# Kernel tuning notes

Hardware: AMD Instinct MI355X
Metric: run time of the kernel (lower is better)

The kernel has to match this reference:

```python
import jax, jax.numpy as jnp
import numpy as np

DIM = 128
HEADS = 8
DH = DIM // HEADS
WIN = (4, 4, 4)
TOPK = 4
EPS = 1e-6


def _ln(x, g, b):
    mu = jnp.mean(x, -1, keepdims=True)
    var = jnp.mean((x - mu) ** 2, -1, keepdims=True)
    return (x - mu) * jax.lax.rsqrt(var + EPS) * g + b


def _win3d(x, p1, p2, p3):
    # x: [B,S,H,W,C] -> [B, p1*p2*p3, Ms, Mh, Mw, C]
    B, S, H, W, C = x.shape
    Ms, Mh, Mw = S // p1, H // p2, W // p3
    x = x.reshape(B, p1, Ms, p2, Mh, p3, Mw, C)
    x = x.transpose(0, 1, 3, 5, 2, 4, 6, 7)
    return x.reshape(B, p1 * p2 * p3, Ms, Mh, Mw, C)


def setup_inputs() -> dict:
    key = jax.random.key(0)
    ks = jax.random.split(key, 20)

    def lin(k, din, dout):
        return jax.random.normal(k, (din, dout), jnp.float32) * 0.02

    return {
        "x_in": jax.random.normal(ks[0], (2, 128, 16, 32, 32), jnp.float32),
        "x_g_in": jax.random.normal(ks[1], (2, 128, 8, 16, 16), jnp.float32),
        # Atten (global branch)
        "qkv_w": lin(ks[2], DIM, 3 * DIM), "qkv_b": jnp.zeros((3 * DIM,), jnp.float32),
        "proj_w": lin(ks[3], DIM, DIM), "proj_b": jnp.zeros((DIM,), jnp.float32),
        # shared LayerNorm (self.norm1 is reused everywhere in the original)
        "ln_g": jnp.ones((DIM,), jnp.float32), "ln_b": jnp.zeros((DIM,), jnp.float32),
        # mlp (global branch FFN)
        "mlp_w1": lin(ks[4], DIM, 4 * DIM), "mlp_b1": jnp.zeros((4 * DIM,), jnp.float32),
        "mlp_w2": lin(ks[5], 4 * DIM, DIM), "mlp_b2": jnp.zeros((DIM,), jnp.float32),
        # TopkRouting
        "rq_w": lin(ks[6], DIM, DIM), "rq_b": jnp.zeros((DIM,), jnp.float32),
        "rk_w": lin(ks[7], DIM, DIM), "rk_b": jnp.zeros((DIM,), jnp.float32),
        # fused qkv over concatenated local+gathered-global tokens
        "gqkv_w": lin(ks[8], DIM, 3 * DIM), "gqkv_b": jnp.zeros((3 * DIM,), jnp.float32),
        "wo_w": lin(ks[9], DIM, DIM), "wo_b": jnp.zeros((DIM,), jnp.float32),
        # mlp2 (local branch FFN)
        "mlp2_w1": lin(ks[10], DIM, 4 * DIM), "mlp2_b1": jnp.zeros((4 * DIM,), jnp.float32),
        "mlp2_w2": lin(ks[11], 4 * DIM, DIM), "mlp2_b2": jnp.zeros((DIM,), jnp.float32),
    }


def reference(x_in, x_g_in, qkv_w, qkv_b, proj_w, proj_b, ln_g, ln_b,
              mlp_w1, mlp_b1, mlp_w2, mlp_b2, rq_w, rq_b, rk_w, rk_b,
              gqkv_w, gqkv_b, wo_w, wo_b, mlp2_w1, mlp2_b1, mlp2_w2, mlp2_b2):
    B, C, S, H, W = x_in.shape
    Ms, Mh, Mw = WIN
    p1, p2, p3 = S // Ms, H // Mh, W // Mw  # pads are zero for these shapes
    nw, w3l = p1 * p2 * p3, Ms * Mh * Mw
    scale = DIM ** -0.5  # BiLevelRoutingAttention.scale = dim**-0.5 (not per-head)

    x = jnp.transpose(x_in, (0, 2, 3, 4, 1))  # [B,S,H,W,C]
    shortcut_l = _win3d(x, p1, p2, p3).reshape(B, nw, w3l, C)

    # ---- global branch: full self-attention + FFN ----
    _, _, gS, gH, gW = x_g_in.shape
    gN = gS * gH * gW
    xg = jnp.transpose(x_g_in, (0, 2, 3, 4, 1)).reshape(B, gN, C)
    h = _ln(xg, ln_g, ln_b)
    qkv = (h @ qkv_w + qkv_b).reshape(B, gN, 3, HEADS, DH).transpose(2, 0, 3, 1, 4)
    q, k, v = qkv[0], qkv[1], qkv[2]
    a = jax.nn.softmax(jnp.einsum('bhnd,bhmd->bhnm', q, k) * DH ** -0.5, axis=-1)
    o = jnp.einsum('bhnm,bhmd->bhnd', a, v).transpose(0, 2, 1, 3).reshape(B, gN, C)
    xg = (o @ proj_w + proj_b) + xg
    xg4 = xg.reshape(B, gS, gH, gW, C)
    h = _ln(xg4, ln_g, ln_b)
    xg4 = xg4 + (jax.nn.gelu(h @ mlp_w1 + mlp_b1, approximate=False) @ mlp_w2 + mlp_b2)

    # ---- top-k window routing ----
    swg = _win3d(xg4, p1, p2, p3)  # [B,nw,gMs,gMh,gMw,C]
    w3g = swg.shape[2] * swg.shape[3] * swg.shape[4]
    g_win = swg.mean((2, 3, 4))  # [B,nw,C]
    qh = g_win @ rq_w + rq_b
    kh = g_win @ rk_w + rk_b
    logit = jnp.einsum('bnc,bmc->bnm', qh * scale, kh)
    _tvals, tidx = jax.lax.top_k(logit, TOPK)  # r_weight is computed but unused in the original forward

    # gather top-k global windows' tokens per local window
    gflat = swg.reshape(B, nw, w3g, C)
    gath = jax.vmap(lambda kv, idx: kv[idx])(gflat, tidx)  # [B,nw,topk,w3g,C]
    sc = jnp.concatenate([shortcut_l, gath.reshape(B, nw, TOPK * w3g, C)], axis=2)
    w3 = w3l + TOPK * w3g

    # ---- local+routed attention over concatenated tokens ----
    qkvp = _ln(sc, ln_g, ln_b) @ gqkv_w + gqkv_b
    qp, kp, vp = jnp.split(qkvp, 3, axis=-1)
    qp = qp.reshape(B, nw, w3, HEADS, DH)
    kp = kp.reshape(B, nw, w3, HEADS, DH)
    vp = vp.reshape(B, nw, w3, HEADS, DH)
    aw = jax.nn.softmax(jnp.einsum('bnqhd,bnkhd->bnhqk', qp * scale, kp), axis=-1)
    out = jnp.einsum('bnhqk,bnkhd->bnqhd', aw, vp).reshape(B, nw, w3, C)

    l = out[:, :, :w3l] @ wo_w + wo_b + shortcut_l
    l = l.reshape(B, p1, p2, p3, Ms, Mh, Mw, C).transpose(0, 1, 4, 2, 5, 3, 6, 7).reshape(B, S, H, W, C)
    l = l + (jax.nn.gelu(_ln(l, ln_g, ln_b) @ mlp2_w1 + mlp2_b1, approximate=False) @ mlp2_w2 + mlp2_b2)

    l_out = jnp.transpose(l, (0, 4, 1, 2, 3))
    g_out = jnp.transpose(xg4, (0, 4, 1, 2, 3))
    return (l_out, g_out)
```

## Files before the change

### kernel.cpp

```cpp
#include <hip/hip_runtime.h>
#include <hip/hip_bf16.h>
#include <math.h>

#define BATCH 2
#define CDIM 128
#define SS 16
#define HH_ 32
#define WW_ 32
#define NSP (SS*HH_*WW_)
#define GS 8
#define GH 16
#define GW 16
#define GN (GS*GH*GW)
#define HEADS 8
#define DH 16
#define NW 256
#define W3L 64
#define W3G 8
#define TOPK 4
#define W3 (W3L + TOPK*W3G)
#define LN_EPS 1e-6f
#define ROUTE_SCALE 0.08838834764831845f
#define GATTN_SCALE 0.25f

typedef short bshort8 __attribute__((ext_vector_type(8)));
typedef float f32x4 __attribute__((ext_vector_type(4)));

__device__ __forceinline__ unsigned short f2bf(float f) {
    unsigned int u = __float_as_uint(f);
    unsigned int r = (u + 0x7fffu + ((u >> 16) & 1u)) >> 16;
    return (unsigned short)r;
}
__device__ __forceinline__ float gelu_exact(float x) {
    float z = x * 0.70710678118654752f;
    float az = fabsf(z);
    float t = 1.0f / fmaf(0.3275911f, az, 1.0f);
    float poly = t * fmaf(t, fmaf(t, fmaf(t, fmaf(t, 1.061405429f, -1.453152027f),
                     1.421413741f), -0.284496736f), 0.254829592f);
    float e = __expf(-az * az);
    float erfv = 1.0f - poly * e;
    erfv = (z < 0.f) ? -erfv : erfv;
    return 0.5f * x * (1.0f + erfv);
}
__device__ __forceinline__ float shfl_sum32(float v) {
#pragma unroll
    for (int m = 16; m > 0; m >>= 1) v += __shfl_xor(v, m);
    return v;
}
__device__ __forceinline__ float shfl_sum16(float v) {
#pragma unroll
    for (int m = 8; m > 0; m >>= 1) v += __shfl_xor(v, m);
    return v;
}
__device__ __forceinline__ float shfl_sum8(float v) {
#pragma unroll
    for (int m = 4; m > 0; m >>= 1) v += __shfl_xor(v, m);
    return v;
}

__global__ __launch_bounds__(256) void k_wprep_all(const float* __restrict__ gqkv_w,
        const float* __restrict__ m2_w1, const float* __restrict__ m2_w2,
        const float* __restrict__ proj_w, const float* __restrict__ mlp_w1,
        const float* __restrict__ mlp_w2, const float* __restrict__ wo_w,
        const float* __restrict__ qkv_w,
        unsigned short* __restrict__ wt, unsigned short* __restrict__ w1t,
        unsigned short* __restrict__ w2t, unsigned short* __restrict__ projt,
        unsigned short* __restrict__ gw1t, unsigned short* __restrict__ gw2t,
        unsigned short* __restrict__ wot, unsigned short* __restrict__ qkvt) {
    int id = blockIdx.x * 256 + threadIdx.x;
    int frag = id >> 6, lane = id & 63;
    int l15 = lane & 15, quad = lane >> 4;
    const float* srcw; unsigned short* dstw; int KS, OUT, lf; float sc = 1.f;
    if (frag < 96)        { lf = frag;       srcw = gqkv_w; dstw = wt;    KS = 4;  OUT = 384; if ((lf >> 2) < 8) sc = ROUTE_SCALE; }
    else if (frag < 224)  { lf = frag - 96;  srcw = m2_w1;  dstw = w1t;   KS = 4;  OUT = 512; }
    else if (frag < 352)  { lf = frag - 224; srcw = m2_w2;  dstw = w2t;   KS = 16; OUT = 128; }
    else if (frag < 384)  { lf = frag - 352; srcw = proj_w; dstw = projt; KS = 4;  OUT = 128; }
    else if (frag < 512)  { lf = frag - 384; srcw = mlp_w1; dstw = gw1t;  KS = 4;  OUT = 512; }
    else if (frag < 640)  { lf = frag - 512; srcw = mlp_w2; dstw = gw2t;  KS = 16; OUT = 128; }
    else if (frag < 672)  { lf = frag - 640; srcw = wo_w;   dstw = wot;   KS = 4;  OUT = 128; }
    else                  { lf = frag - 672; srcw = qkv_w;  dstw = qkvt;  KS = 4;  OUT = 384; if ((lf >> 2) < 8) sc = GATTN_SCALE; }
    int ksh = (KS == 16) ? 4 : 2;
    int tile = lf >> ksh, ks = lf & (KS - 1);
    int n = tile * 16 + l15;
    int k0 = ks * 32 + quad * 8;
    const float* s = srcw + (size_t)k0 * OUT + n;
    unsigned short o[8];
#pragma unroll
    for (int e = 0; e < 8; e++) o[e] = f2bf(s[(size_t)e * OUT] * sc);
    unsigned short* d = dstw + ((size_t)lf * 64 + lane) * 8;
    *(ushort4*)d = *(ushort4*)&o[0];
    *(ushort4*)(d + 4) = *(ushort4*)&o[4];
}

__global__ __launch_bounds__(256) void k_gqkv_mfma(const float* __restrict__ xg_in,
        const unsigned short* __restrict__ qkvt, const float* __restrict__ qkv_b,
        const float* __restrict__ ln_g, const float* __restrict__ ln_b,
        float* __restrict__ xg, unsigned short* __restrict__ qgb,
        unsigned short* __restrict__ kgb, unsigned short* __restrict__ vgtb) {
    int blk = blockIdx.x; int b = blk >> 7; int n0 = (blk & 127) * 16;
    int t = threadIdx.x; int w = t >> 6; int lane = t & 63;
    int l15 = lane & 15, quad = lane >> 4;
    __shared__ __align__(16) float xs[16 * 132];
    __shared__ __align__(16) unsigned short h[16 * 136];
    f32x4 zero4 = {0.f, 0.f, 0.f, 0.f};

    {
        int c = t >> 1, j0 = (t & 1) * 8;
        const float* src = xg_in + ((size_t)(b * 128 + c)) * GN + n0 + j0;
        float4 v0 = *(const float4*)src;
        float4 v1 = *(const float4*)(src + 4);
        xs[(j0 + 0) * 132 + c] = v0.x; xs[(j0 + 1) * 132 + c] = v0.y;
        xs[(j0 + 2) * 132 + c] = v0.z; xs[(j0 + 3) * 132 + c] = v0.w;
        xs[(j0 + 4) * 132 + c] = v1.x; xs[(j0 + 5) * 132 + c] = v1.y;
        xs[(j0 + 6) * 132 + c] = v1.z; xs[(j0 + 7) * 132 + c] = v1.w;
    }
    __syncthreads();
    {
        int j = t >> 4, p = t & 15, c0 = p * 8;
        float vv[8]; float s1 = 0.f;
#pragma unroll
        for (int i = 0; i < 8; i++) { vv[i] = xs[j * 132 + c0 + i]; s1 += vv[i]; }
        s1 = shfl_sum16(s1);
        float mu = s1 * (1.0f / 128.0f);
        float s2 = 0.f;
#pragma unroll
        for (int i = 0; i < 8; i++) { float d = vv[i] - mu; s2 += d * d; }
        s2 = shfl_sum16(s2);
        float rs = rsqrtf(s2 * (1.0f / 128.0f) + LN_EPS);
        float* dst = xg + ((size_t)(b * GN) + n0 + j) * 128 + c0;
        *(float4*)dst = *(float4*)&vv[0];
        *(float4*)(dst + 4) = *(float4*)&vv[4];
        unsigned short hb[8];
#pragma unroll
        for (int i4 = 0; i4 < 2; i4++) {
            float4 g4 = *(const float4*)(ln_g + c0 + i4 * 4);
            float4 b4 = *(const float4*)(ln_b + c0 + i4 * 4);
            hb[i4 * 4 + 0] = f2bf((vv[i4 * 4 + 0] - mu) * rs * g4.x + b4.x);
            hb[i4 * 4 + 1] = f2bf((vv[i4 * 4 + 1] - mu) * rs * g4.y + b4.y);
            hb[i4 * 4 + 2] = f2bf((vv[i4 * 4 + 2] - mu) * rs * g4.z + b4.z);
            hb[i4 * 4 + 3] = f2bf((vv[i4 * 4 + 3] - mu) * rs * g4.w + b4.w);
        }
        *(ushort4*)&h[j * 136 + c0] = *(ushort4*)&hb[0];
        *(ushort4*)&h[j * 136 + c0 + 4] = *(ushort4*)&hb[4];
    }
    __syncthreads();

    bshort8 a[4];
#pragma unroll
    for (int ks = 0; ks < 4; ks++)
        a[ks] = *(const bshort8*)(h + l15 * 136 + ks * 32 + quad * 8);
    int bh_base = b * HEADS;
#pragma unroll
    for (int part = 0; part < 2; part++) {
#pragma unroll
        for (int which = 0; which < 2; which++) {
            int nt = 2 * w + which;
            f32x4 acc = zero4;
#pragma unroll
            for (int ks = 0; ks < 4; ks++) {
                bshort8 bfr = *(const bshort8*)(qkvt + (((size_t)(part * 8 + nt) * 4 + ks) * 64 + lane) * 8);
                acc = __builtin_amdgcn_mfma_f32_16x16x32_bf16(a[ks], bfr, acc, 0, 0, 0);
            }
            int ncol = part * 128 + nt * 16;
            float bias = qkv_b[ncol + l15] * (part == 0 ? GATTN_SCALE : 1.f);
            unsigned short* dst = (part == 0) ? qgb : kgb;
#pragma unroll
            for (int r = 0; r < 4; r++)
                dst[((size_t)(bh_base + nt) * GN + n0 + quad * 4 + r) * DH + l15] = f2bf(acc[r] + bias);
        }
    }
#pragma unroll
    for (int which = 0; which < 2; which++) {
        int mtv = 2 * w + which;
        f32x4 acc = zero4;
#pragma unroll
        for (int ks = 0; ks < 4; ks++) {
            bshort8 aw = *(const bshort8*)(qkvt + (((size_t)(16 + mtv) * 4 + ks) * 64 + lane) * 8);
            acc = __builtin_amdgcn_mfma_f32_16x16x32_bf16(aw, a[ks], acc, 0, 0, 0);
        }
#pragma unroll
        for (int r = 0; r < 4; r++) {
            float bias = qkv_b[256 + mtv * 16 + quad * 4 + r];
            vgtb[((size_t)(bh_base + mtv) * DH + quad * 4 + r) * GN + n0 + l15] = f2bf(acc[r] + bias);
        }
    }
}

__global__ __launch_bounds__(256) void k_gattn_mfma(const unsigned short* __restrict__ qgb,
        const unsigned short* __restrict__ kgb, const unsigned short* __restrict__ vgtb,
        float* __restrict__ og) {
    int blk = blockIdx.x;
    int bh = blk >> 7; int qt = (blk & 127) << 4;
    int b = bh >> 3, hh = bh & 7;
    int t = threadIdx.x; int w = t >> 6; int lane = t & 63;
    int col = lane & 15, quad = lane >> 4;
    __shared__ __align__(16) unsigned short Pbuf[4 * 16 * 40];
    __shared__ float po[4][64][4];
    __shared__ float pl[4][64][4];

    bshort8 aq = {0, 0, 0, 0, 0, 0, 0, 0};
    if (quad < 2)
        aq = *(const bshort8*)(qgb + ((size_t)bh * GN + qt + col) * DH + quad * 8);

    f32x4 o = {0.f, 0.f, 0.f, 0.f};
    float lsum[4] = {0.f, 0.f, 0.f, 0.f};
    const unsigned short* kb = kgb + (size_t)bh * GN * DH;
    const unsigned short* vb = vgtb + (size_t)bh * DH * GN;
    unsigned short* pb = Pbuf + w * (16 * 40);
    int row0 = quad * 4;
    int kbeg = w * 512;
    for (int kc = kbeg; kc < kbeg + 512; kc += 32) {
        bshort8 bk0 = {0, 0, 0, 0, 0, 0, 0, 0};
        bshort8 bk1 = {0, 0, 0, 0, 0, 0, 0, 0};
        if (quad < 2) {
            bk0 = *(const bshort8*)(kb + (size_t)(kc + col) * DH + quad * 8);
            bk1 = *(const bshort8*)(kb + (size_t)(kc + 16 + col) * DH + quad * 8);
        }
        f32x4 z = {0.f, 0.f, 0.f, 0.f};
        f32x4 s0 = __builtin_amdgcn_mfma_f32_16x16x32_bf16(aq, bk0, z, 0, 0, 0);
        f32x4 s1 = __builtin_amdgcn_mfma_f32_16x16x32_bf16(aq, bk1, z, 0, 0, 0);
        float p0[4], p1[4];
#pragma unroll
        for (int r = 0; r < 4; r++) {
            p0[r] = __expf(s0[r]); p1[r] = __expf(s1[r]);
            lsum[r] += p0[r] + p1[r];
        }
#pragma unroll
        for (int r = 0; r < 4; r++) {
            pb[(row0 + r) * 40 + col] = f2bf(p0[r]);
            pb[(row0 + r) * 40 + 16 + col] = f2bf(p1[r]);
        }
        bshort8 pA = *(const bshort8*)(pb + col * 40 + quad * 8);
        bshort8 bv = *(const bshort8*)(vb + (size_t)col * GN + kc + quad * 8);
        o = __builtin_amdgcn_mfma_f32_16x16x32_bf16(pA, bv, o, 0, 0, 0);
    }
#pragma unroll
    for (int r = 0; r < 4; r++) {
        float v = lsum[r];
        v += __shfl_xor(v, 1); v += __shfl_xor(v, 2);
        v += __shfl_xor(v, 4); v += __shfl_xor(v, 8);
        lsum[r] = v;
    }
#pragma unroll
    for (int r = 0; r < 4; r++) { po[w][lane][r] = o[r]; pl[w][lane][r] = lsum[r]; }
    __syncthreads();
    if (w == 0) {
#pragma unroll
        for (int r = 0; r < 4; r++) {
            float os = po[0][lane][r] + po[1][lane][r] + po[2][lane][r] + po[3][lane][r];
            float ls = pl[0][lane][r] + pl[1][lane][r] + pl[2][lane][r] + pl[3][lane][r];
            og[((size_t)(b * GN) + qt + quad * 4 + r) * 128 + hh * 16 + col] = os / ls;
        }
    }
}

__global__ __launch_bounds__(256) void k_gmlp_mfma(const float* __restrict__ og,
        const float* __restrict__ xg,
        const unsigned short* __restrict__ projt, const float* __restrict__ proj_b,
        const float* __restrict__ ln_g, const float* __restrict__ ln_b,
        const unsigned short* __restrict__ gw1t, const float* __restrict__ b1,
        const unsigned short* __restrict__ gw2t, const float* __restrict__ b2,
        float* __restrict__ xg4, float* __restrict__ gout) {
    int blk = blockIdx.x; int b = blk >> 7; int n0g = (blk & 127) * 16;
    int t = threadIdx.x; int w = t >> 6; int lane = t & 63;
    int l15 = lane & 15, quad = lane >> 4;
    __shared__ __align__(16) unsigned short ao[16 * 136];
    __shared__ __align__(16) float xs[16 * 132];
    __shared__ __align__(16) unsigned short h[16 * 136];
    __shared__ __align__(16) unsigned short h1[16 * 520];
    float* of32 = (float*)h1;
    f32x4 zero4 = {0.f, 0.f, 0.f, 0.f};

    {
        int j = t >> 4, p = t & 15, c0 = p * 8;
        size_t base = ((size_t)(b * GN) + n0g + j) * 128 + c0;
        float4 v0 = *(const float4*)(og + base);
        float4 v1 = *(const float4*)(og + base + 4);
        ushort4 u0 = { f2bf(v0.x), f2bf(v0.y), f2bf(v0.z), f2bf(v0.w) };
        ushort4 u1 = { f2bf(v1.x), f2bf(v1.y), f2bf(v1.z), f2bf(v1.w) };
        *(ushort4*)&ao[j * 136 + c0] = u0;
        *(ushort4*)&ao[j * 136 + c0 + 4] = u1;
        *(float4*)&xs[j * 132 + c0] = *(const float4*)(xg + base);
        *(float4*)&xs[j * 132 + c0 + 4] = *(const float4*)(xg + base + 4);
    }
    __syncthreads();

    {
        bshort8 a[4];
#pragma unroll
        for (int ks = 0; ks < 4; ks++)
            a[ks] = *(const bshort8*)(ao + l15 * 136 + ks * 32 + quad * 8);
#pragma unroll
        for (int nt = 0; nt < 2; nt++) {
            f32x4 acc = zero4;
#pragma unroll
            for (int ks = 0; ks < 4; ks++) {
                bshort8 bfr = *(const bshort8*)(projt + (((size_t)(w * 2 + nt) * 4 + ks) * 64 + lane) * 8);
                acc = __builtin_amdgcn_mfma_f32_16x16x32_bf16(a[ks], bfr, acc, 0, 0, 0);
            }
            int n0 = w * 32 + nt * 16;
            float bias = proj_b[n0 + l15];
#pragma unroll
            for (int r = 0; r < 4; r++) {
                int m = quad * 4 + r;
                xs[m * 132 + n0 + l15] += acc[r] + bias;
            }
        }
    }
    __syncthreads();

    {
        int j = t >> 4, p = t & 15, c0 = p * 8;
        float vv[8]; float s1 = 0.f;
#pragma unroll
        for (int i = 0; i < 8; i++) { vv[i] = xs[j * 132 + c0 + i]; s1 += vv[i]; }
        s1 = shfl_sum16(s1);
        float mu = s1 * (1.0f / 128.0f);
        float s2 = 0.f;
#pragma unroll
        for (int i = 0; i < 8; i++) { float d = vv[i] - mu; s2 += d * d; }
        s2 = shfl_sum16(s2);
        float rs = rsqrtf(s2 * (1.0f / 128.0f) + LN_EPS);
        unsigned short hb[8];
#pragma unroll
        for (int i4 = 0; i4 < 2; i4++) {
            float4 g4 = *(const float4*)(ln_g + c0 + i4 * 4);
            float4 b4 = *(const float4*)(ln_b + c0 + i4 * 4);
            hb[i4 * 4 + 0] = f2bf((vv[i4 * 4 + 0] - mu) * rs * g4.x + b4.x);
            hb[i4 * 4 + 1] = f2bf((vv[i4 * 4 + 1] - mu) * rs * g4.y + b4.y);
            hb[i4 * 4 + 2] = f2bf((vv[i4 * 4 + 2] - mu) * rs * g4.z + b4.z);
            hb[i4 * 4 + 3] = f2bf((vv[i4 * 4 + 3] - mu) * rs * g4.w + b4.w);
        }
        *(ushort4*)&h[j * 136 + c0] = *(ushort4*)&hb[0];
        *(ushort4*)&h[j * 136 + c0 + 4] = *(ushort4*)&hb[4];
    }
    __syncthreads();

    {
        bshort8 a[4];
#pragma unroll
        for (int ks = 0; ks < 4; ks++)
            a[ks] = *(const bshort8*)(h + l15 * 136 + ks * 32 + quad * 8);
#pragma unroll
        for (int nt = 0; nt < 8; nt++) {
            f32x4 acc = zero4;
#pragma unroll
            for (int ks = 0; ks < 4; ks++) {
                bshort8 bfr = *(const bshort8*)(gw1t + (((size_t)(w * 8 + nt) * 4 + ks) * 64 + lane) * 8);
                acc = __builtin_amdgcn_mfma_f32_16x16x32_bf16(a[ks], bfr, acc, 0, 0, 0);
            }
            int n0 = w * 128 + nt * 16;
            float bias = b1[n0 + l15];
#pragma unroll
            for (int r = 0; r < 4; r++)
                h1[(quad * 4 + r) * 520 + n0 + l15] = f2bf(gelu_exact(acc[r] + bias));
        }
    }
    __syncthreads();

    f32x4 acc2[2]; acc2[0] = zero4; acc2[1] = zero4;
#pragma unroll 4
    for (int ks = 0; ks < 16; ks++) {
        bshort8 a = *(const bshort8*)(h1 + l15 * 520 + ks * 32 + quad * 8);
#pragma unroll
        for (int nt = 0; nt < 2; nt++) {
            bshort8 bfr = *(const bshort8*)(gw2t + (((size_t)(w * 2 + nt) * 16 + ks) * 64 + lane) * 8);
            acc2[nt] = __builtin_amdgcn_mfma_f32_16x16x32_bf16(a, bfr, acc2[nt], 0, 0, 0);
        }
    }
    __syncthreads();

    {
#pragma unroll
        for (int nt = 0; nt < 2; nt++) {
            int n0 = w * 32 + nt * 16;
            float bias = b2[n0 + l15];
#pragma unroll
            for (int r = 0; r < 4; r++) {
                int m = quad * 4 + r;
                float ov = xs[m * 132 + n0 + l15] + acc2[nt][r] + bias;
                of32[m * 132 + n0 + l15] = ov;
                xg4[((size_t)(b * GN) + n0g + m) * 128 + n0 + l15] = ov;
            }
        }
    }
    __syncthreads();

    {
        int cw = t >> 1, hf = t & 1, j0 = hf * 8;
        float* dst = gout + ((size_t)(b * 128 + cw)) * GN + n0g + j0;
#pragma unroll
        for (int i4 = 0; i4 < 2; i4++) {
            float4 ov = { of32[(j0 + i4 * 4 + 0) * 132 + cw], of32[(j0 + i4 * 4 + 1) * 132 + cw],
                          of32[(j0 + i4 * 4 + 2) * 132 + cw], of32[(j0 + i4 * 4 + 3) * 132 + cw] };
            *(float4*)(dst + i4 * 4) = ov;
        }
    }
}

__global__ void k_routing_qk(const float* __restrict__ xg4,
                             const float* __restrict__ rq_w, const float* __restrict__ rq_b,
                             const float* __restrict__ rk_w, const float* __restrict__ rk_b,
                             float* __restrict__ qh, float* __restrict__ kh) {
    int wid = blockIdx.x; int b = wid / NW, n = wid % NW;
    int c = threadIdx.x;
    int i1 = n / 64, i2 = (n / 8) % 8, i3 = n % 8;
    __shared__ float g[CDIM];
    float s = 0.f;
#pragma unroll
    for (int j = 0; j < W3G; j++) {
        int ds = j >> 2, dh = (j >> 1) & 1, dw = j & 1;
        int gi = ((i1 * 2 + ds) * GH + (i2 * 2 + dh)) * GW + (i3 * 2 + dw);
        s += xg4[((size_t)(b * GN + gi)) * CDIM + c];
    }
    g[c] = s * (1.0f / W3G);
    __syncthreads();
    float aq = rq_b[c], ak = rk_b[c];
    for (int k = 0; k < CDIM; k++) { float gv = g[k]; aq = fmaf(gv, rq_w[k * CDIM + c], aq); ak = fmaf(gv, rk_w[k * CDIM + c], ak); }
    qh[(size_t)wid * CDIM + c] = aq;
    kh[(size_t)wid * CDIM + c] = ak;
}

__global__ void k_topk(const float* __restrict__ qh, const float* __restrict__ kh,
                       int* __restrict__ tidx) {
    int wid = blockIdx.x; int b = wid / NW;
    int m = threadIdx.x;
    __shared__ float q[CDIM];
    __shared__ float lv[NW];
    __shared__ int li[NW];
    if (m < CDIM) q[m] = qh[(size_t)wid * CDIM + m] * ROUTE_SCALE;
    __syncthreads();
    float acc = 0.f;
    const float* kr = kh + ((size_t)b * NW + m) * CDIM;
    for (int k = 0; k < CDIM; k++) acc = fmaf(q[k], kr[k], acc);
#pragma unroll
    for (int sel = 0; sel < TOPK; sel++) {
        lv[m] = acc; li[m] = m; __syncthreads();
#pragma unroll
        for (int s = 128; s > 0; s >>= 1) {
            if (m < s) {
                if (lv[m + s] > lv[m] || (lv[m + s] == lv[m] && li[m + s] < li[m])) {
                    lv[m] = lv[m + s]; li[m] = li[m + s];
                }
            }
            __syncthreads();
        }
        int best = li[0]; __syncthreads();
        if (m == best) acc = -1e30f;
        if (m == 0) tidx[wid * TOPK + sel] = best;
    }
}

__global__ __launch_bounds__(256) void k_lnsc_local(const float* __restrict__ x_in,
        const float* __restrict__ ln_g, const float* __restrict__ ln_b,
        unsigned short* __restrict__ lnsc) {
    int blk = blockIdx.x;
    int wt = blk & 1; int hh = (blk >> 1) & 31; int s = (blk >> 6) & 15; int b = blk >> 10;
    int w0 = wt * 16;
    int t = threadIdx.x;
    __shared__ float tile[16][132];
    {
        int c = t >> 1; int wq = (t & 1) * 8;
        const float* src = x_in + (((size_t)(b * 128 + c) * SS + s)) * 1024 + hh * 32 + w0 + wq;
        float4 v0 = *(const float4*)src;
        float4 v1 = *(const float4*)(src + 4);
        tile[wq + 0][c] = v0.x; tile[wq + 1][c] = v0.y; tile[wq + 2][c] = v0.z; tile[wq + 3][c] = v0.w;
        tile[wq + 4][c] = v1.x; tile[wq + 5][c] = v1.y; tile[wq + 6][c] = v1.z; tile[wq + 7][c] = v1.w;
    }
    __syncthreads();
    int w = t >> 4; int j = t & 15;
    float vals[8];
    float s1 = 0.f;
#pragma unroll
    for (int i = 0; i < 8; i++) { vals[i] = tile[w][j * 8 + i]; s1 += vals[i]; }
    s1 = shfl_sum16(s1);
    float mu = s1 * (1.0f / 128.0f);
    float s2 = 0.f;
#pragma unroll
    for (int i = 0; i < 8; i++) { float d = vals[i] - mu; s2 += d * d; }
    s2 = shfl_sum16(s2);
    float rs = rsqrtf(s2 * (1.0f / 128.0f) + LN_EPS);
    float4 g0 = *(const float4*)(ln_g + j * 8);
    float4 g1 = *(const float4*)(ln_g + j * 8 + 4);
    float4 b0 = *(const float4*)(ln_b + j * 8);
    float4 b1 = *(const float4*)(ln_b + j * 8 + 4);
    float gv[8] = { g0.x, g0.y, g0.z, g0.w, g1.x, g1.y, g1.z, g1.w };
    float bv[8] = { b0.x, b0.y, b0.z, b0.w, b1.x, b1.y, b1.z, b1.w };
    int ww = w0 + w;
    int n = (s >> 2) * 64 + (hh >> 2) * 8 + (ww >> 2);
    int slot = (s & 3) * 16 + (hh & 3) * 4 + (ww & 3);
    unsigned short* dst = lnsc + ((size_t)(b * NW + n) * W3 + slot) * 128 + j * 8;
    ushort4 u0, u1;
    u0.x = f2bf((vals[0] - mu) * rs * gv[0] + bv[0]);
    u0.y = f2bf((vals[1] - mu) * rs * gv[1] + bv[1]);
    u0.z = f2bf((vals[2] - mu) * rs * gv[2] + bv[2]);
    u0.w = f2bf((vals[3] - mu) * rs * gv[3] + bv[3]);
    u1.x = f2bf((vals[4] - mu) * rs * gv[4] + bv[4]);
    u1.y = f2bf((vals[5] - mu) * rs * gv[5] + bv[5]);
    u1.z = f2bf((vals[6] - mu) * rs * gv[6] + bv[6]);
    u1.w = f2bf((vals[7] - mu) * rs * gv[7] + bv[7]);
    *(ushort4*)dst = u0;
    *(ushort4*)(dst + 4) = u1;
}

__global__ __launch_bounds__(256) void k_lnsc_gath(const float* __restrict__ xg4,
        const int* __restrict__ tidx,
        const float* __restrict__ ln_g, const float* __restrict__ ln_b,
        unsigned short* __restrict__ lnsc) {
    int blk = blockIdx.x;
    int kk = blk & 3; int wn = blk >> 2;
    int b = wn >> 8;
    int g = tidx[wn * TOPK + kk];
    int gi1 = g >> 6, gi2 = (g >> 3) & 7, gi3 = g & 7;
    int t = threadIdx.x; int j = t >> 5, lj = t & 31;
    int ds = j >> 2, dh = (j >> 1) & 1, dw = j & 1;
    int gi = ((gi1 * 2 + ds) * GH + (gi2 * 2 + dh)) * GW + (gi3 * 2 + dw);
    float4 v = *(const float4*)(xg4 + ((size_t)(b * GN + gi)) * 128 + lj * 4);
    float s1 = shfl_sum32(v.x + v.y + v.z + v.w);
    float mu = s1 * (1.0f / 128.0f);
    float d0 = v.x - mu, d1 = v.y - mu, d2 = v.z - mu, d3 = v.w - mu;
    float s2 = shfl_sum32(d0 * d0 + d1 * d1 + d2 * d2 + d3 * d3);
    float rs = rsqrtf(s2 * (1.0f / 128.0f) + LN_EPS);
    float4 g4 = *(const float4*)(ln_g + lj * 4);
    float4 b4 = *(const float4*)(ln_b + lj * 4);
    ushort4 u;
    u.x = f2bf(d0 * rs * g4.x + b4.x);
    u.y = f2bf(d1 * rs * g4.y + b4.y);
    u.z = f2bf(d2 * rs * g4.z + b4.z);
    u.w = f2bf(d3 * rs * g4.w + b4.w);
    *(ushort4*)(lnsc + ((size_t)wn * W3 + 64 + kk * 8 + j) * 128 + lj * 4) = u;
}

__global__ __launch_bounds__(512, 4) void k_local_mfma(const unsigned short* __restrict__ lnsc,
        const unsigned short* __restrict__ wt, const float* __restrict__ gqkv_b,
        float* __restrict__ aout) {
    int wn = blockIdx.x;
    int t = threadIdx.x; int w = t >> 6; int lane = t & 63;
    int l15 = lane & 15, quad = lane >> 4;
    __shared__ __align__(16) unsigned short Qs[64 * 136];
    __shared__ __align__(16) unsigned short Ks2[96 * 136];
    __shared__ __align__(16) unsigned short Vts[128 * 104];
    __shared__ __align__(16) unsigned short Ps[8][16 * 40];

    const unsigned short* Xb = lnsc + (size_t)wn * W3 * 128;
    f32x4 zero4 = {0.f, 0.f, 0.f, 0.f};

    bshort8 qw[4], kw[4], vw[4];
#pragma unroll
    for (int ks = 0; ks < 4; ks++) {
        qw[ks] = *(const bshort8*)(wt + (((size_t)(0 + w) * 4 + ks) * 64 + lane) * 8);
        kw[ks] = *(const bshort8*)(wt + (((size_t)(8 + w) * 4 + ks) * 64 + lane) * 8);
        vw[ks] = *(const bshort8*)(wt + (((size_t)(16 + w) * 4 + ks) * 64 + lane) * 8);
    }
    float qbias = gqkv_b[w * 16 + l15] * ROUTE_SCALE;
    float kbias = gqkv_b[128 + w * 16 + l15];
    float vbias[4];
#pragma unroll
    for (int r = 0; r < 4; r++) vbias[r] = gqkv_b[256 + w * 16 + quad * 4 + r];

    for (int mt = 0; mt < 6; mt++) {
        bshort8 a[4];
#pragma unroll
        for (int ks = 0; ks < 4; ks++)
            a[ks] = *(const bshort8*)(Xb + (mt * 16 + l15) * 128 + ks * 32 + quad * 8);
        f32x4 acck = zero4;
        f32x4 accv = zero4;
#pragma unroll
        for (int ks = 0; ks < 4; ks++) {
            acck = __builtin_amdgcn_mfma_f32_16x16x32_bf16(a[ks], kw[ks], acck, 0, 0, 0);
            accv = __builtin_amdgcn_mfma_f32_16x16x32_bf16(vw[ks], a[ks], accv, 0, 0, 0);
        }
#pragma unroll
        for (int r = 0; r < 4; r++) {
            Ks2[(mt * 16 + quad * 4 + r) * 136 + w * 16 + l15] = f2bf(acck[r] + kbias);
            Vts[(w * 16 + quad * 4 + r) * 104 + mt * 16 + l15] = f2bf(accv[r] + vbias[r]);
        }
        if (mt < 4) {
            f32x4 accq = zero4;
#pragma unroll
            for (int ks = 0; ks < 4; ks++)
                accq = __builtin_amdgcn_mfma_f32_16x16x32_bf16(a[ks], qw[ks], accq, 0, 0, 0);
#pragma unroll
            for (int r = 0; r < 4; r++)
                Qs[(mt * 16 + quad * 4 + r) * 136 + w * 16 + l15] = f2bf(accq[r] + qbias);
        }
    }

    unsigned short* Pw = &Ps[w][0];
    bshort8 zfrag = {0, 0, 0, 0, 0, 0, 0, 0};
    int h = w;
    for (int mt = 0; mt < 4; mt++) {
        bshort8 aq = zfrag;
        if (quad < 2)
            aq = *(const bshort8*)(Qs + (mt * 16 + l15) * 136 + h * 16 + quad * 8);
        float rsum[4] = {0.f, 0.f, 0.f, 0.f};
        f32x4 oacc = zero4;
#pragma unroll
        for (int kc = 0; kc < 96; kc += 32) {
#pragma unroll
            for (int sub = 0; sub < 2; sub++) {
                int nt = (kc >> 4) + sub;
                bshort8 bk = zfrag;
                if (quad < 2)
                    bk = *(const bshort8*)(Ks2 + (nt * 16 + l15) * 136 + h * 16 + quad * 8);
                f32x4 s = __builtin_amdgcn_mfma_f32_16x16x32_bf16(aq, bk, zero4, 0, 0, 0);
#pragma unroll
                for (int r = 0; r < 4; r++) {
                    float p = __expf(s[r]);
                    rsum[r] += p;
                    Pw[(quad * 4 + r) * 40 + sub * 16 + l15] = f2bf(p);
                }
            }
            bshort8 ap = *(const bshort8*)(Pw + l15 * 40 + quad * 8);
            bshort8 bv = *(const bshort8*)(Vts + (h * 16 + l15) * 104 + kc + quad * 8);
            oacc = __builtin_amdgcn_mfma_f32_16x16x32_bf16(ap, bv, oacc, 0, 0, 0);
        }
#pragma unroll
        for (int r = 0; r < 4; r++) {
            float v = rsum[r];
            v += __shfl_xor(v, 1); v += __shfl_xor(v, 2);
            v += __shfl_xor(v, 4); v += __shfl_xor(v, 8);
            rsum[r] = v;
        }
#pragma unroll
        for (int r = 0; r < 4; r++)
            aout[((size_t)wn * W3L + mt * 16 + quad * 4 + r) * 128 + h * 16 + l15]
                = oacc[r] / rsum[r];
    }
}

__global__ __launch_bounds__(256) void k_wo_mfma(const float* __restrict__ aout,
        const unsigned short* __restrict__ wot, const float* __restrict__ wo_b,
        const float* __restrict__ x_in, float* __restrict__ lpre) {
    int blk = blockIdx.x; int T0 = blk * 32;
    int b = T0 >> 14; int sp0 = T0 & 16383;
    int t = threadIdx.x; int w = t >> 6; int lane = t & 63;
    int l15 = lane & 15, quad = lane >> 4;
    __shared__ __align__(16) unsigned short as2[32 * 136];
    __shared__ __align__(16) float xs[32 * 132];
    f32x4 zero4 = {0.f, 0.f, 0.f, 0.f};

    {
        int j = t >> 3, p = t & 7, c0 = p * 16;
        int sp = sp0 + j;
        int s = sp >> 10, hh = (sp >> 5) & 31, ww = sp & 31;
        int n = (s >> 2) * 64 + (hh >> 2) * 8 + (ww >> 2);
        int slot = (s & 3) * 16 + (hh & 3) * 4 + (ww & 3);
        const float* src = aout + (((size_t)(b * NW + n)) * W3L + slot) * 128 + c0;
#pragma unroll
        for (int i4 = 0; i4 < 4; i4++) {
            float4 v = *(const float4*)(src + i4 * 4);
            ushort4 u = { f2bf(v.x), f2bf(v.y), f2bf(v.z), f2bf(v.w) };
            *(ushort4*)&as2[j * 136 + c0 + i4 * 4] = u;
        }
    }
    {
        int c = t >> 1, half = t & 1, j0 = half * 16;
        const float* src = x_in + ((size_t)(b * 128 + c)) * 16384 + sp0 + j0;
#pragma unroll
        for (int i4 = 0; i4 < 4; i4++) {
            float4 v = *(const float4*)(src + i4 * 4);
            xs[(j0 + i4 * 4 + 0) * 132 + c] = v.x;
            xs[(j0 + i4 * 4 + 1) * 132 + c] = v.y;
            xs[(j0 + i4 * 4 + 2) * 132 + c] = v.z;
            xs[(j0 + i4 * 4 + 3) * 132 + c] = v.w;
        }
    }
    __syncthreads();

    bshort8 a[2][4];
#pragma unroll
    for (int mt = 0; mt < 2; mt++)
#pragma unroll
        for (int ks = 0; ks < 4; ks++)
            a[mt][ks] = *(const bshort8*)(as2 + (mt * 16 + l15) * 136 + ks * 32 + quad * 8);
#pragma unroll
    for (int nt = 0; nt < 2; nt++) {
        int n0 = w * 32 + nt * 16;
        f32x4 acc0 = zero4, acc1 = zero4;
#pragma unroll
        for (int ks = 0; ks < 4; ks++) {
            bshort8 bfr = *(const bshort8*)(wot + (((size_t)(w * 2 + nt) * 4 + ks) * 64 + lane) * 8);
            acc0 = __builtin_amdgcn_mfma_f32_16x16x32_bf16(a[0][ks], bfr, acc0, 0, 0, 0);
            acc1 = __builtin_amdgcn_mfma_f32_16x16x32_bf16(a[1][ks], bfr, acc1, 0, 0, 0);
        }
        float bias = wo_b[n0 + l15];
#pragma unroll
        for (int r = 0; r < 4; r++) {
            int m0 = quad * 4 + r;
            int m1 = 16 + quad * 4 + r;
            lpre[((size_t)T0 + m0) * 128 + n0 + l15] = acc0[r] + bias + xs[m0 * 132 + n0 + l15];
            lpre[((size_t)T0 + m1) * 128 + n0 + l15] = acc1[r] + bias + xs[m1 * 132 + n0 + l15];
        }
    }
}

__global__ __launch_bounds__(256) void k_mlp2_mfma(const float* __restrict__ lpre,
        const float* __restrict__ ln_g, const float* __restrict__ ln_b,
        const unsigned short* __restrict__ w1t, const float* __restrict__ b1,
        const unsigned short* __restrict__ w2t, const float* __restrict__ b2,
        float* __restrict__ lout) {
    int blk = blockIdx.x;
    int T0 = blk * 32;
    int b = T0 >> 14;
    int sp = T0 & 16383;
    int t = threadIdx.x; int w = t >> 6; int lane = t & 63;
    int l15 = lane & 15, quad = lane >> 4;
    __shared__ __align__(16) unsigned short buf[32 * 520];
    float* of32 = (float*)buf;

    float res[2][2][4];
#pragma unroll
    for (int mt = 0; mt < 2; mt++)
#pragma unroll
        for (int nt = 0; nt < 2; nt++)
#pragma unroll
            for (int r = 0; r < 4; r++)
                res[mt][nt][r] = lpre[((size_t)T0 + mt * 16 + quad * 4 + r) * 128 + w * 32 + nt * 16 + l15];

    {
        int j = t >> 3, p = t & 7, c0 = p * 16;
        const float* src = lpre + ((size_t)T0 + j) * 128 + c0;
        float4 v0 = *(const float4*)(src + 0);
        float4 v1 = *(const float4*)(src + 4);
        float4 v2 = *(const float4*)(src + 8);
        float4 v3 = *(const float4*)(src + 12);
        float s1 = (v0.x + v0.y + v0.z + v0.w) + (v1.x + v1.y + v1.z + v1.w)
                 + (v2.x + v2.y + v2.z + v2.w) + (v3.x + v3.y + v3.z + v3.w);
        s1 = shfl_sum8(s1);
        float mu = s1 * (1.0f / 128.0f);
        float vv[16] = { v0.x, v0.y, v0.z, v0.w, v1.x, v1.y, v1.z, v1.w,
                         v2.x, v2.y, v2.z, v2.w, v3.x, v3.y, v3.z, v3.w };
        float s2 = 0.f;
#pragma unroll
        for (int i = 0; i < 16; i++) { float d = vv[i] - mu; s2 += d * d; }
        s2 = shfl_sum8(s2);
        float rs = rsqrtf(s2 * (1.0f / 128.0f) + LN_EPS);
        unsigned short hb[16];
#pragma unroll
        for (int i4 = 0; i4 < 4; i4++) {
            float4 g4 = *(const float4*)(ln_g + c0 + i4 * 4);
            float4 b4 = *(const float4*)(ln_b + c0 + i4 * 4);
            hb[i4 * 4 + 0] = f2bf((vv[i4 * 4 + 0] - mu) * rs * g4.x + b4.x);
            hb[i4 * 4 + 1] = f2bf((vv[i4 * 4 + 1] - mu) * rs * g4.y + b4.y);
            hb[i4 * 4 + 2] = f2bf((vv[i4 * 4 + 2] - mu) * rs * g4.z + b4.z);
            hb[i4 * 4 + 3] = f2bf((vv[i4 * 4 + 3] - mu) * rs * g4.w + b4.w);
        }
        *(ushort4*)&buf[j * 136 + c0 + 0] = *(ushort4*)&hb[0];
        *(ushort4*)&buf[j * 136 + c0 + 4] = *(ushort4*)&hb[4];
        *(ushort4*)&buf[j * 136 + c0 + 8] = *(ushort4*)&hb[8];
        *(ushort4*)&buf[j * 136 + c0 + 12] = *(ushort4*)&hb[12];
    }
    __syncthreads();

    bshort8 a1[2][4];
#pragma unroll
    for (int mt = 0; mt < 2; mt++)
#pragma unroll
        for (int ks = 0; ks < 4; ks++)
            a1[mt][ks] = *(const bshort8*)(buf + (mt * 16 + l15) * 136 + ks * 32 + quad * 8);
    __syncthreads();

    f32x4 zero4 = {0.f, 0.f, 0.f, 0.f};
    {
#pragma unroll
        for (int nt = 0; nt < 8; nt++) {
            int n0 = w * 128 + nt * 16;
            f32x4 acc0 = zero4, acc1 = zero4;
#pragma unroll
            for (int ks = 0; ks < 4; ks++) {
                bshort8 bfr = *(const bshort8*)(w1t + (((size_t)(w * 8 + nt) * 4 + ks) * 64 + lane) * 8);
                acc0 = __builtin_amdgcn_mfma_f32_16x16x32_bf16(a1[0][ks], bfr, acc0, 0, 0, 0);
                acc1 = __builtin_amdgcn_mfma_f32_16x16x32_bf16(a1[1][ks], bfr, acc1, 0, 0, 0);
            }
            float bias = b1[n0 + l15];
#pragma unroll
            for (int r = 0; r < 4; r++) {
                buf[(quad * 4 + r) * 520 + n0 + l15] = f2bf(gelu_exact(acc0[r] + bias));
                buf[(16 + quad * 4 + r) * 520 + n0 + l15] = f2bf(gelu_exact(acc1[r] + bias));
            }
        }
    }
    __syncthreads();

    f32x4 acc[2][2];
    acc[0][0] = zero4; acc[0][1] = zero4; acc[1][0] = zero4; acc[1][1] = zero4;
    {
#pragma unroll 4
        for (int ks = 0; ks < 16; ks++) {
            bshort8 a0 = *(const bshort8*)(buf + (l15) * 520 + ks * 32 + quad * 8);
            bshort8 a1b = *(const bshort8*)(buf + (16 + l15) * 520 + ks * 32 + quad * 8);
#pragma unroll
            for (int nt = 0; nt < 2; nt++) {
                bshort8 bfr = *(const bshort8*)(w2t + (((size_t)(w * 2 + nt) * 16 + ks) * 64 + lane) * 8);
                acc[0][nt] = __builtin_amdgcn_mfma_f32_16x16x32_bf16(a0, bfr, acc[0][nt], 0, 0, 0);
                acc[1][nt] = __builtin_amdgcn_mfma_f32_16x16x32_bf16(a1b, bfr, acc[1][nt], 0, 0, 0);
            }
        }
    }
    __syncthreads();

#pragma unroll
    for (int mt = 0; mt < 2; mt++) {
#pragma unroll
        for (int nt = 0; nt < 2; nt++) {
            int n0 = w * 32 + nt * 16;
            float bias = b2[n0 + l15];
#pragma unroll
            for (int r = 0; r < 4; r++) {
                int m = mt * 16 + quad * 4 + r;
                of32[m * 132 + n0 + l15] = res[mt][nt][r] + acc[mt][nt][r] + bias;
            }
        }
    }
    __syncthreads();

    {
        int c = t >> 1, half = t & 1, j0 = half * 16;
        float* dst = lout + ((size_t)(b * 128 + c)) * NSP + sp + j0;
#pragma unroll
        for (int i4 = 0; i4 < 4; i4++) {
            float4 ov = { of32[(j0 + i4 * 4 + 0) * 132 + c], of32[(j0 + i4 * 4 + 1) * 132 + c],
                          of32[(j0 + i4 * 4 + 2) * 132 + c], of32[(j0 + i4 * 4 + 3) * 132 + c] };
            *(float4*)(dst + i4 * 4) = ov;
        }
    }
}

extern "C" void kernel_launch(void* const* d_in, const int* in_sizes, int n_in,
                              void* d_out, int out_size, void* d_ws, size_t ws_size,
                              hipStream_t stream) {
    const float* x_in   = (const float*)d_in[0];
    const float* xg_in  = (const float*)d_in[1];
    const float* qkv_w  = (const float*)d_in[2];
    const float* qkv_b  = (const float*)d_in[3];
    const float* proj_w = (const float*)d_in[4];
    const float* proj_b = (const float*)d_in[5];
    const float* ln_g   = (const float*)d_in[6];
    const float* ln_b   = (const float*)d_in[7];
    const float* mlp_w1 = (const float*)d_in[8];
    const float* mlp_b1 = (const float*)d_in[9];
    const float* mlp_w2 = (const float*)d_in[10];
    const float* mlp_b2 = (const float*)d_in[11];
    const float* rq_w   = (const float*)d_in[12];
    const float* rq_b   = (const float*)d_in[13];
    const float* rk_w   = (const float*)d_in[14];
    const float* rk_b   = (const float*)d_in[15];
    const float* gqkv_w = (const float*)d_in[16];
    const float* gqkv_b = (const float*)d_in[17];
    const float* wo_w   = (const float*)d_in[18];
    const float* wo_b   = (const float*)d_in[19];
    const float* m2_w1  = (const float*)d_in[20];
    const float* m2_b1  = (const float*)d_in[21];
    const float* m2_w2  = (const float*)d_in[22];
    const float* m2_b2  = (const float*)d_in[23];

    float* out = (float*)d_out;
    float* ws  = (float*)d_ws;

    float* xg4 = ws;
    float* xg  = ws + 524288;
    unsigned short* qgb  = (unsigned short*)(ws + 1048576);
    unsigned short* kgb  = (unsigned short*)(ws + 1310720);
    unsigned short* vgtb = (unsigned short*)(ws + 1572864);
    float* og  = ws + 1835008;
    float* qh  = ws + 2359296;
    float* kh  = ws + 2424832;
    int*   tidx = (int*)(ws + 2490368);
    unsigned short* lnsc = (unsigned short*)(ws + 2492416);
    float* aout = ws + 2492416 + 3145728;
    float* lpre = ws + 9832448;
    unsigned short* wt   = (unsigned short*)(ws + 14026752);
    unsigned short* w1t  = (unsigned short*)(ws + 14051328);
    unsigned short* w2t  = (unsigned short*)(ws + 14084096);
    unsigned short* projt = (unsigned short*)(ws + 14116864);
    unsigned short* gw1t  = (unsigned short*)(ws + 14125056);
    unsigned short* gw2t  = (unsigned short*)(ws + 14157824);
    unsigned short* wot   = (unsigned short*)(ws + 14190592);
    unsigned short* qkvt  = (unsigned short*)(ws + 14198784);

    const size_t L_OUT = (size_t)BATCH * CDIM * NSP;
    float* gout = out + L_OUT;

    hipLaunchKernelGGL(k_wprep_all, dim3(192), dim3(256), 0, stream,
                       gqkv_w, m2_w1, m2_w2, proj_w, mlp_w1, mlp_w2, wo_w, qkv_w,
                       wt, w1t, w2t, projt, gw1t, gw2t, wot, qkvt);
    hipLaunchKernelGGL(k_gqkv_mfma, dim3(256), dim3(256), 0, stream,
                       xg_in, qkvt, qkv_b, ln_g, ln_b, xg, qgb, kgb, vgtb);
    hipLaunchKernelGGL(k_gattn_mfma, dim3(2048), dim3(256), 0, stream, qgb, kgb, vgtb, og);
    hipLaunchKernelGGL(k_gmlp_mfma, dim3(256), dim3(256), 0, stream,
                       og, xg, projt, proj_b, ln_g, ln_b, gw1t, mlp_b1, gw2t, mlp_b2,
                       xg4, gout);
    hipLaunchKernelGGL(k_routing_qk, dim3(512), dim3(128), 0, stream,
                       xg4, rq_w, rq_b, rk_w, rk_b, qh, kh);
    hipLaunchKernelGGL(k_topk, dim3(512), dim3(256), 0, stream, qh, kh, tidx);
    hipLaunchKernelGGL(k_lnsc_local, dim3(2048), dim3(256), 0, stream,
                       x_in, ln_g, ln_b, lnsc);
    hipLaunchKernelGGL(k_lnsc_gath, dim3(2048), dim3(256), 0, stream,
                       xg4, tidx, ln_g, ln_b, lnsc);
    hipLaunchKernelGGL(k_local_mfma, dim3(512), dim3(512), 0, stream,
                       lnsc, wt, gqkv_b, aout);
    hipLaunchKernelGGL(k_wo_mfma, dim3(1024), dim3(256), 0, stream,
                       aout, wot, wo_b, x_in, lpre);
    hipLaunchKernelGGL(k_mlp2_mfma, dim3(1024), dim3(256), 0, stream,
                       lpre, ln_g, ln_b, w1t, m2_b1, w2t, m2_b2, out);
}
```

Before: 248.0 us.

## Fuse output projection and residual into local attention kernel

The wo projection, bias and residual add are merged into the local attention kernel. Attention output stays in shared memory as bf16, reusing the Q buffer, instead of being written to global as fp32 and read back by a separate kernel. x_in residual values are prefetched into registers early and staged through the K buffer region. This removes one kernel launch and a global round trip of the attention output, at the cost of more registers and an extra block barrier in the attention kernel.

```diff
diff --git a/kernel.cpp b/kernel.cpp
--- a/kernel.cpp
+++ b/kernel.cpp
@@ -531,19 +531,35 @@
     *(ushort4*)(lnsc + ((size_t)wn * W3 + 64 + kk * 8 + j) * 128 + lj * 4) = u;
 }
 
-__global__ __launch_bounds__(512, 4) void k_local_mfma(const unsigned short* __restrict__ lnsc,
+__global__ __launch_bounds__(512, 4) void k_local_wo_mfma(const unsigned short* __restrict__ lnsc,
         const unsigned short* __restrict__ wt, const float* __restrict__ gqkv_b,
-        float* __restrict__ aout) {
+        const unsigned short* __restrict__ wot, const float* __restrict__ wo_b,
+        const float* __restrict__ x_in, float* __restrict__ lpre) {
     int wn = blockIdx.x;
+    int b = wn >> 8; int n = wn & 255;
+    int i1 = n >> 6, i2 = (n >> 3) & 7, i3 = n & 7;
+    int s0 = i1 * 4, h0 = i2 * 4, w0 = i3 * 4;
     int t = threadIdx.x; int w = t >> 6; int lane = t & 63;
     int l15 = lane & 15, quad = lane >> 4;
-    __shared__ __align__(16) unsigned short Qs[64 * 136];
-    __shared__ __align__(16) unsigned short Ks2[96 * 136];
-    __shared__ __align__(16) unsigned short Vts[128 * 104];
-    __shared__ __align__(16) unsigned short Ps[8][16 * 40];
+    __shared__ __align__(16) unsigned short SMEM[64 * 136 + 96 * 136 + 128 * 104 + 8 * 640];
+    unsigned short* Qs  = SMEM;
+    unsigned short* Ks2 = SMEM + 64 * 136;
+    unsigned short* Vts = SMEM + 64 * 136 + 96 * 136;
+    unsigned short* Ps  = SMEM + 64 * 136 + 96 * 136 + 128 * 104;
+    float* xs = (float*)Ks2;
 
     const unsigned short* Xb = lnsc + (size_t)wn * W3 * 128;
     f32x4 zero4 = {0.f, 0.f, 0.f, 0.f};
+
+    int cx = t >> 2, sub = t & 3;
+    float4 xr[4];
+#pragma unroll
+    for (int i = 0; i < 4; i++) {
+        int jr = sub * 4 + i;
+        int ds = jr >> 2, dh = jr & 3;
+        xr[i] = *(const float4*)(x_in + ((size_t)(b * 128 + cx)) * 16384
+                                 + (size_t)(s0 + ds) * 1024 + (h0 + dh) * 32 + w0);
+    }
 
     bshort8 qw[4], kw[4], vw[4];
 #pragma unroll
@@ -586,7 +602,7 @@
         }
     }
 
-    unsigned short* Pw = &Ps[w][0];
+    unsigned short* Pw = Ps + w * 640;
     bshort8 zfrag = {0, 0, 0, 0, 0, 0, 0, 0};
     int h = w;
     for (int mt = 0; mt < 4; mt++) {
@@ -598,8 +614,8 @@
 #pragma unroll
         for (int kc = 0; kc < 96; kc += 32) {
 #pragma unroll
-            for (int sub = 0; sub < 2; sub++) {
-                int nt = (kc >> 4) + sub;
+            for (int sub2 = 0; sub2 < 2; sub2++) {
+                int nt = (kc >> 4) + sub2;
                 bshort8 bk = zfrag;
                 if (quad < 2)
                     bk = *(const bshort8*)(Ks2 + (nt * 16 + l15) * 136 + h * 16 + quad * 8);
@@ -608,7 +624,7 @@
                 for (int r = 0; r < 4; r++) {
                     float p = __expf(s[r]);
                     rsum[r] += p;
-                    Pw[(quad * 4 + r) * 40 + sub * 16 + l15] = f2bf(p);
+                    Pw[(quad * 4 + r) * 40 + sub2 * 16 + l15] = f2bf(p);
                 }
             }
             bshort8 ap = *(const bshort8*)(Pw + l15 * 40 + quad * 8);
@@ -624,73 +640,42 @@
         }
 #pragma unroll
         for (int r = 0; r < 4; r++)
-            aout[((size_t)wn * W3L + mt * 16 + quad * 4 + r) * 128 + h * 16 + l15]
-                = oacc[r] / rsum[r];
-    }
-}
-
-__global__ __launch_bounds__(256) void k_wo_mfma(const float* __restrict__ aout,
-        const unsigned short* __restrict__ wot, const float* __restrict__ wo_b,
-        const float* __restrict__ x_in, float* __restrict__ lpre) {
-    int blk = blockIdx.x; int T0 = blk * 32;
-    int b = T0 >> 14; int sp0 = T0 & 16383;
-    int t = threadIdx.x; int w = t >> 6; int lane = t & 63;
-    int l15 = lane & 15, quad = lane >> 4;
-    __shared__ __align__(16) unsigned short as2[32 * 136];
-    __shared__ __align__(16) float xs[32 * 132];
-    f32x4 zero4 = {0.f, 0.f, 0.f, 0.f};
-
-    {
-        int j = t >> 3, p = t & 7, c0 = p * 16;
-        int sp = sp0 + j;
-        int s = sp >> 10, hh = (sp >> 5) & 31, ww = sp & 31;
-        int n = (s >> 2) * 64 + (hh >> 2) * 8 + (ww >> 2);
-        int slot = (s & 3) * 16 + (hh & 3) * 4 + (ww & 3);
-        const float* src = aout + (((size_t)(b * NW + n)) * W3L + slot) * 128 + c0;
-#pragma unroll
-        for (int i4 = 0; i4 < 4; i4++) {
-            float4 v = *(const float4*)(src + i4 * 4);
-            ushort4 u = { f2bf(v.x), f2bf(v.y), f2bf(v.z), f2bf(v.w) };
-            *(ushort4*)&as2[j * 136 + c0 + i4 * 4] = u;
-        }
-    }
-    {
-        int c = t >> 1, half = t & 1, j0 = half * 16;
-        const float* src = x_in + ((size_t)(b * 128 + c)) * 16384 + sp0 + j0;
-#pragma unroll
-        for (int i4 = 0; i4 < 4; i4++) {
-            float4 v = *(const float4*)(src + i4 * 4);
-            xs[(j0 + i4 * 4 + 0) * 132 + c] = v.x;
-            xs[(j0 + i4 * 4 + 1) * 132 + c] = v.y;
-            xs[(j0 + i4 * 4 + 2) * 132 + c] = v.z;
-            xs[(j0 + i4 * 4 + 3) * 132 + c] = v.w;
-        }
-    }
-    __syncthreads();
-
-    bshort8 a[2][4];
-#pragma unroll
-    for (int mt = 0; mt < 2; mt++)
+            Qs[(mt * 16 + quad * 4 + r) * 136 + h * 16 + l15] = f2bf(oacc[r] / rsum[r]);
+    }
+
+    __syncthreads();
+
+#pragma unroll
+    for (int i = 0; i < 4; i++) {
+        int jr = sub * 4 + i;
+        xs[(jr * 4 + 0) * 132 + cx] = xr[i].x;
+        xs[(jr * 4 + 1) * 132 + cx] = xr[i].y;
+        xs[(jr * 4 + 2) * 132 + cx] = xr[i].z;
+        xs[(jr * 4 + 3) * 132 + cx] = xr[i].w;
+    }
+
+    float wbias = wo_b[w * 16 + l15];
+    bshort8 wow[4];
+#pragma unroll
+    for (int ks = 0; ks < 4; ks++)
+        wow[ks] = *(const bshort8*)(wot + (((size_t)w * 4 + ks) * 64 + lane) * 8);
+#pragma unroll
+    for (int mt = 0; mt < 4; mt++) {
+        bshort8 a[4];
 #pragma unroll
         for (int ks = 0; ks < 4; ks++)
-            a[mt][ks] = *(const bshort8*)(as2 + (mt * 16 + l15) * 136 + ks * 32 + quad * 8);
-#pragma unroll
-    for (int nt = 0; nt < 2; nt++) {
-        int n0 = w * 32 + nt * 16;
-        f32x4 acc0 = zero4, acc1 = zero4;
-#pragma unroll
-        for (int ks = 0; ks < 4; ks++) {
-            bshort8 bfr = *(const bshort8*)(wot + (((size_t)(w * 2 + nt) * 4 + ks) * 64 + lane) * 8);
-            acc0 = __builtin_amdgcn_mfma_f32_16x16x32_bf16(a[0][ks], bfr, acc0, 0, 0, 0);
-            acc1 = __builtin_amdgcn_mfma_f32_16x16x32_bf16(a[1][ks], bfr, acc1, 0, 0, 0);
-        }
-        float bias = wo_b[n0 + l15];
+            a[ks] = *(const bshort8*)(Qs + (mt * 16 + l15) * 136 + ks * 32 + quad * 8);
+        f32x4 acc = zero4;
+#pragma unroll
+        for (int ks = 0; ks < 4; ks++)
+            acc = __builtin_amdgcn_mfma_f32_16x16x32_bf16(a[ks], wow[ks], acc, 0, 0, 0);
 #pragma unroll
         for (int r = 0; r < 4; r++) {
-            int m0 = quad * 4 + r;
-            int m1 = 16 + quad * 4 + r;
-            lpre[((size_t)T0 + m0) * 128 + n0 + l15] = acc0[r] + bias + xs[m0 * 132 + n0 + l15];
-            lpre[((size_t)T0 + m1) * 128 + n0 + l15] = acc1[r] + bias + xs[m1 * 132 + n0 + l15];
+            int slot = mt * 16 + quad * 4 + r;
+            int ds = slot >> 4, dh = (slot >> 2) & 3, dw = slot & 3;
+            int sp = (s0 + ds) * 1024 + (h0 + dh) * 32 + (w0 + dw);
+            lpre[((size_t)(b * 16384) + sp) * 128 + w * 16 + l15]
+                = acc[r] + wbias + xs[slot * 132 + w * 16 + l15];
         }
     }
 }
@@ -868,8 +853,7 @@
     float* kh  = ws + 2424832;
     int*   tidx = (int*)(ws + 2490368);
     unsigned short* lnsc = (unsigned short*)(ws + 2492416);
-    float* aout = ws + 2492416 + 3145728;
-    float* lpre = ws + 9832448;
+    float* lpre = ws + 2492416 + 3145728;
     unsigned short* wt   = (unsigned short*)(ws + 14026752);
     unsigned short* w1t  = (unsigned short*)(ws + 14051328);
     unsigned short* w2t  = (unsigned short*)(ws + 14084096);
@@ -898,10 +882,8 @@
                        x_in, ln_g, ln_b, lnsc);
     hipLaunchKernelGGL(k_lnsc_gath, dim3(2048), dim3(256), 0, stream,
                        xg4, tidx, ln_g, ln_b, lnsc);
-    hipLaunchKernelGGL(k_local_mfma, dim3(512), dim3(512), 0, stream,
-                       lnsc, wt, gqkv_b, aout);
-    hipLaunchKernelGGL(k_wo_mfma, dim3(1024), dim3(256), 0, stream,
-                       aout, wot, wo_b, x_in, lpre);
+    hipLaunchKernelGGL(k_local_wo_mfma, dim3(512), dim3(512), 0, stream,
+                       lnsc, wt, gqkv_b, wot, wo_b, x_in, lpre);
     hipLaunchKernelGGL(k_mlp2_mfma, dim3(1024), dim3(256), 0, stream,
                        lpre, ln_g, ln_b, w1t, m2_b1, w2t, m2_b2, out);
 }
```

New measurement: 250.3 us. About the same (+0.9%).
